# Performance work log

Measured on AMD Instinct MI355X. Metric: run time of the kernel, lower is better.

The kernel has to match this reference:

```python
import jax, jax.numpy as jnp
import numpy as np


def build_mask_even(kh, kw):
    # Hexnet build_masks: zero one edge column for kernel rows at odd distance
    # from the kernel center (hex neighborhood); returns even-row mask + shift.
    mask = np.ones((kh, kw), dtype=np.float32)
    center = kh // 2
    shift = -1 if center % 2 else 1
    for r in range(kh):
        if abs(center - r) % 2:
            if shift == 1:
                mask[r, -1] = 0.0
            else:
                mask[r, 0] = 0.0
    return mask, shift


def setup_inputs() -> dict:
    key = jax.random.key(0)
    k1, k2, k3 = jax.random.split(key, 3)
    x = jax.random.normal(k1, (16, 128, 128, 128), dtype=jnp.float32)  # NHWC
    kernel = jax.random.normal(k2, (3, 3, 128, 256), dtype=jnp.float32) * 0.05  # HWIO
    bias = jax.random.normal(k3, (256,), dtype=jnp.float32) * 0.05
    return {"x": x, "kernel": kernel, "bias": bias}


def _hconv(x, kernel, bias):
    kh, kw = kernel.shape[0], kernel.shape[1]
    mask_np, shift = build_mask_even(kh, kw)
    kernel_even = kernel * jnp.asarray(mask_np)[:, :, None, None]

    # Odd-row kernel: only the rows at odd distance from center, rolled along width.
    center = kh // 2
    odd_rows = [jnp.roll(kernel_even[r], shift, axis=0)
                for r in range(kh) if abs(center - r) % 2]
    kernel_odd = jnp.stack(odd_rows, axis=0)  # (n_odd, kw, Cin, F)

    dn = ("NHWC", "HWIO", "NHWC")
    strides = (2, 1)  # build() doubles the H stride
    out_even = jax.lax.conv_general_dilated(
        x, kernel_even, window_strides=strides, padding="SAME",
        dimension_numbers=dn)
    out_odd = jax.lax.conv_general_dilated(
        x[:, 1:], kernel_odd, window_strides=strides, padding="SAME",
        dimension_numbers=dn)

    # Interleave rows: even0, odd0, even1, odd1, ... (+ trailing even row if longer)
    he, ho = out_even.shape[1], out_odd.shape[1]
    hm = min(he, ho)
    b, _, w, f = out_even.shape
    out = jnp.stack([out_even[:, :hm], out_odd[:, :hm]], axis=2)
    out = out.reshape(b, 2 * hm, w, f)
    if he > ho:
        out = jnp.concatenate([out, out_even[:, -1:]], axis=1)

    return jax.nn.relu(out + bias)


def reference(x, kernel, bias):
    return _hconv(x, kernel, bias)
```

## Files before the change

### kernel.cpp

```cpp
#include <hip/hip_runtime.h>


#define N_  16
#define H_  128
#define W_  128
#define C_  128
#define F_  256
#define HP  130
#define WP  130

#define A_TILE_B   16640
#define B_SLOT_B   16384
#define B_BASE     A_TILE_B

typedef short bf16x8 __attribute__((ext_vector_type(8)));
typedef float f32x4  __attribute__((ext_vector_type(4)));

__device__ __forceinline__ unsigned int bf_bits(float f) {
  unsigned int u = __float_as_uint(f);
  return (u + 0x7FFFu + ((u >> 16) & 1u)) >> 16;
}
__device__ __forceinline__ unsigned int pack2(float a, float b) {
  return bf_bits(a) | (bf_bits(b) << 16);
}

__device__ __forceinline__ void even_tap(int ti, int& dr, int& dc, int& kr, int& kc) {
  switch (ti) {
    case 0:  dr = 0; dc = 0;  kr = 0; kc = 1; break;
    case 1:  dr = 0; dc = 1;  kr = 0; kc = 2; break;
    case 2:  dr = 1; dc = -1; kr = 1; kc = 0; break;
    case 3:  dr = 1; dc = 0;  kr = 1; kc = 1; break;
    case 4:  dr = 1; dc = 1;  kr = 1; kc = 2; break;
    case 5:  dr = 2; dc = 0;  kr = 2; kc = 1; break;
    default: dr = 2; dc = 1;  kr = 2; kc = 2; break;
  }
}

__global__ __launch_bounds__(256) void prep_xpadH(
    const float* __restrict__ x, char* __restrict__ xp) {
  long id = (long)blockIdx.x * 256 + threadIdx.x;
  const int g  = (int)(id & 7);
  const int hc = (int)((id >> 3) & 1);
  long pix = id >> 4;
  const int wp = (int)(pix % WP);
  long t = pix / WP;
  const int hh = (int)(t % HP);
  const int nn = (int)(t / HP);
  const int ww = wp - 1;
  uint4 o = make_uint4(0u, 0u, 0u, 0u);
  if (hh < H_ && ww >= 0 && ww < W_) {
    const float* s = x + (((long)(nn * H_ + hh) * W_ + ww) * C_ + hc * 64 + ((g ^ (wp & 7)) * 8));
    float4 a = *(const float4*)s;
    float4 b = *(const float4*)(s + 4);
    o.x = pack2(a.x, a.y); o.y = pack2(a.z, a.w);
    o.z = pack2(b.x, b.y); o.w = pack2(b.z, b.w);
  }
  *(uint4*)(xp + id * 16) = o;
}

__global__ __launch_bounds__(256) void prep_wt2(
    const float* __restrict__ k, char* __restrict__ wt2) {
  int id = blockIdx.x * 256 + threadIdx.x;
  if (id >= 7 * 2 * 2 * 128 * 8) return;
  const int g  = id & 7;
  const int f  = (id >> 3) & 127;
  const int ft = (id >> 10) & 1;
  const int hc = (id >> 11) & 1;
  const int ti = id >> 12;
  int dr, dc, kr, kc;
  even_tap(ti, dr, dc, kr, kc);
  const int fg = ft * 128 + f;
  const int c0 = hc * 64 + (g ^ (f & 7)) * 8;
  float v[8];
#pragma unroll
  for (int j = 0; j < 8; ++j)
    v[j] = k[((size_t)(kr * 3 + kc) * C_ + (c0 + j)) * F_ + fg];
  uint4 o;
  o.x = pack2(v[0], v[1]); o.y = pack2(v[2], v[3]);
  o.z = pack2(v[4], v[5]); o.w = pack2(v[6], v[7]);
  *(uint4*)(wt2 + (size_t)id * 16) = o;
}

__global__ __launch_bounds__(256, 3) void hconv_mfma(
    const char* __restrict__ xpadH,
    const char* __restrict__ wt2,
    const float* __restrict__ bias,
    float* __restrict__ out) {
  __shared__ __align__(16) char smem[49408];

  const int tid = threadIdx.x;
  const int bid = (blockIdx.x & 7) * 512 + (blockIdx.x >> 3);
  const int ft = bid & 1;
  const int h  = (bid >> 1) & 127;
  const int n  = bid >> 8;
  const int p  = h & 1;
  const int nsteps = p ? 8 : 14;

  const int lane = tid & 63;
  const int wid  = tid >> 6;
  const int wr   = wid >> 1;
  const int wc   = wid & 1;
  const int l16  = lane & 15;
  const int lk   = lane >> 4;

  auto step_info = [&](int s, int& dc, int& widx, int& dr, int& hc) {
    if (p == 0) {
      hc = (s >= 7);
      const int tap = hc ? s - 7 : s;
      int kr, kc; even_tap(tap, dr, dc, kr, kc);
      widx = tap;
    } else {
      hc = (s >= 4);
      const int j = s & 3;
      dr = j >> 1;
      dc = (j & 1) ? 0 : -1;
      widx = (j == 0) ? 0 : (j == 1) ? 1 : (j == 2) ? 5 : 6;
    }
  };
  auto tile_of = [&](int s) {
    if (p == 0) {
      const int hcp = (s >= 7);
      const int tap = hcp ? s - 7 : s;
      const int grp = (tap < 2) ? 0 : (tap < 5) ? 1 : 2;
      return hcp * 3 + grp;
    } else {
      return s >> 1;
    }
  };

  auto stageA = [&](int tile) {
    int dr, hc;
    if (p == 0) { hc = tile >= 3; const int g3 = hc ? tile - 3 : tile; dr = g3; }
    else        { hc = tile >= 2; dr = tile & 1; }
    const long pixb = (long)(n * HP + (h + dr)) * WP;
#pragma unroll
    for (int i = 0; i < 5; ++i) {
      const int L = i * 256 + tid;
      if (L < 1040) {
        const int wp = L >> 3, g = L & 7;
        const char* src = xpadH + ((pixb + wp) * 2 + hc) * 128 + g * 16;
        __builtin_amdgcn_global_load_lds(
            (const __attribute__((address_space(1))) void*)src,
            (__attribute__((address_space(3))) void*)((char*)smem + L * 16), 16, 0, 0);
      }
    }
  };
  auto stageB = [&](int s, int sel) {
    int dc, widx, dr, hc; step_info(s, dc, widx, dr, hc);
    const char* bsrc = wt2 + (size_t)((widx * 2 + hc) * 2 + ft) * 16384;
    char* base = (char*)smem + B_BASE + sel * B_SLOT_B;
#pragma unroll
    for (int i = 0; i < 4; ++i) {
      const int L = i * 256 + tid;
      __builtin_amdgcn_global_load_lds(
          (const __attribute__((address_space(1))) void*)(bsrc + L * 16),
          (__attribute__((address_space(3))) void*)(base + L * 16), 16, 0, 0);
    }
  };

  f32x4 acc[4][4] = {};

  stageA(0);
  stageB(0, 0);
  __syncthreads();

  int cur = 0;
  for (int s = 0; s < nsteps; ++s) {
    int dc, widx, dr, hc; step_info(s, dc, widx, dr, hc);
    const char* ab = (const char*)smem;
    const char* bb = (const char*)smem + B_BASE + cur * B_SLOT_B;

    bf16x8 af[4][2], bfr[4][2];
#pragma unroll
    for (int m = 0; m < 4; ++m) {
      const int wp = wr * 64 + m * 16 + l16 + dc + 1;
      const int key = wp & 7;
#pragma unroll
      for (int kk = 0; kk < 2; ++kk)
        af[m][kk] = *(const bf16x8*)(ab + wp * 128 + (((kk * 4 + lk) ^ key) * 16));
    }
#pragma unroll
    for (int fi = 0; fi < 4; ++fi) {
      const int fl = wc * 64 + fi * 16 + l16;
#pragma unroll
      for (int kk = 0; kk < 2; ++kk)
        bfr[fi][kk] = *(const bf16x8*)(bb + fl * 128 + (((kk * 4 + lk) ^ (fl & 7)) * 16));
    }

    if (s + 1 < nsteps) stageB(s + 1, cur ^ 1);

#pragma unroll
    for (int m = 0; m < 4; ++m)
#pragma unroll
      for (int fi = 0; fi < 4; ++fi)
#pragma unroll
        for (int kk = 0; kk < 2; ++kk)
          acc[m][fi] = __builtin_amdgcn_mfma_f32_16x16x32_bf16(
              af[m][kk], bfr[fi][kk], acc[m][fi], 0, 0, 0);

    if (s + 1 < nsteps) {
      if (tile_of(s + 1) != tile_of(s)) {
        __syncthreads();
        stageA(tile_of(s + 1));
      }
      __syncthreads();
      cur ^= 1;
    }
  }

#pragma unroll
  for (int fi = 0; fi < 4; ++fi) {
    const int f = ft * 128 + wc * 64 + fi * 16 + l16;
    const float bv = bias[f];
#pragma unroll
    for (int m = 0; m < 4; ++m) {
      const int w = wr * 64 + m * 16 + lk * 4;
      float* o = out + (((size_t)(n * H_ + h) * W_ + w) * F_ + f);
#pragma unroll
      for (int r = 0; r < 4; ++r) {
        float v = acc[m][fi][r] + bv;
        v = v > 0.f ? v : 0.f;
        o[(size_t)r * F_] = v;
      }
    }
  }
}

__device__ __forceinline__ void tap_info11(int t, int& dr, int& dc, int& kr, int& kc) {
  switch (t) {
    case 0:  dr = 0; dc = 0;  kr = 0; kc = 1; break;
    case 1:  dr = 0; dc = 1;  kr = 0; kc = 2; break;
    case 2:  dr = 1; dc = -1; kr = 1; kc = 0; break;
    case 3:  dr = 1; dc = 0;  kr = 1; kc = 1; break;
    case 4:  dr = 1; dc = 1;  kr = 1; kc = 2; break;
    case 5:  dr = 2; dc = 0;  kr = 2; kc = 1; break;
    case 6:  dr = 2; dc = 1;  kr = 2; kc = 2; break;
    case 7:  dr = 0; dc = -1; kr = 0; kc = 1; break;
    case 8:  dr = 0; dc = 0;  kr = 0; kc = 2; break;
    case 9:  dr = 1; dc = -1; kr = 2; kc = 1; break;
    default: dr = 1; dc = 0;  kr = 2; kc = 2; break;
  }
}

__global__ __launch_bounds__(256) void build_w_fb(
    const float* __restrict__ k, unsigned short* __restrict__ wt) {
  int tid = blockIdx.x * 256 + threadIdx.x;
  if (tid >= 11 * F_ * C_) return;
  int c = tid & 127;
  int f = (tid >> 7) & 255;
  int t = tid >> 15;
  int dr, dc, kr, kc;
  tap_info11(t, dr, dc, kr, kc);
  wt[tid] = (unsigned short)bf_bits(k[((kr * 3 + kc) * C_ + c) * F_ + f]);
}

__global__ __launch_bounds__(256, 3) void hconv_fb(
    const float* __restrict__ x,
    const unsigned short* __restrict__ wt,
    const float* __restrict__ bias,
    float* __restrict__ out) {
  __shared__ __align__(16) char smem_s[49152];
  const int tid = threadIdx.x;
  const int bid = (blockIdx.x & 7) * 1024 + (blockIdx.x >> 3);
  const int ft    = bid & 1;
  const int wtile = (bid >> 1) & 1;
  const int h     = (bid >> 2) & 127;
  const int n     = bid >> 9;
  const int f0 = ft * 128;
  const int w0 = wtile * 64;
  const int p  = h & 1;
  const int tap0   = p ? 7 : 0;
  const int nsteps = p ? 8 : 14;
  const int lane = tid & 63;
  const int wid  = tid >> 6;
  const int l16  = lane & 15;
  const int lk   = lane >> 4;
  const int awl = tid >> 2;
  const int ag2 = tid & 3;
  const int bfl   = tid >> 1;
  const int bhalf = tid & 1;
  float4 ar0, ar1, ar2, ar3;
  uint4  br0, br1, br2, br3;
  auto load_step = [&](int s) {
    const int tap = tap0 + (s >> 1);
    const int cc  = s & 1;
    int dr, dc, kr, kc;
    tap_info11(tap, dr, dc, kr, kc);
    const int hh = h + dr;
    const int wg = w0 + awl + dc;
    const bool av = (hh < H_) && (wg >= 0) && (wg < W_);
    if (av) {
      const float* ap = x + (((long)(n * H_ + hh) * W_ + wg) * C_ + cc * 64 + ag2 * 16);
      ar0 = *(const float4*)(ap);
      ar1 = *(const float4*)(ap + 4);
      ar2 = *(const float4*)(ap + 8);
      ar3 = *(const float4*)(ap + 12);
    } else {
      ar0 = ar1 = ar2 = ar3 = make_float4(0.f, 0.f, 0.f, 0.f);
    }
    const unsigned short* bp =
        wt + ((size_t)(tap * F_ + f0 + bfl) * C_ + cc * 64 + bhalf * 32);
    const uint4* bq = (const uint4*)bp;
    br0 = bq[0]; br1 = bq[1]; br2 = bq[2]; br3 = bq[3];
  };
  auto write_step = [&](int sel) {
    uint4 u0, u1;
    u0.x = pack2(ar0.x, ar0.y); u0.y = pack2(ar0.z, ar0.w);
    u0.z = pack2(ar1.x, ar1.y); u0.w = pack2(ar1.z, ar1.w);
    u1.x = pack2(ar2.x, ar2.y); u1.y = pack2(ar2.z, ar2.w);
    u1.z = pack2(ar3.x, ar3.y); u1.w = pack2(ar3.z, ar3.w);
    char* abase = (char*)smem_s + sel * 8192 + awl * 128;
    const int sw = awl & 7;
    *(uint4*)(abase + (((2 * ag2)     ^ sw) * 16)) = u0;
    *(uint4*)(abase + (((2 * ag2 + 1) ^ sw) * 16)) = u1;
    char* bbase = (char*)smem_s + 16384 + sel * 16384 + bfl * 128;
    const int sb = bfl & 7;
    *(uint4*)(bbase + (((bhalf * 4 + 0) ^ sb) * 16)) = br0;
    *(uint4*)(bbase + (((bhalf * 4 + 1) ^ sb) * 16)) = br1;
    *(uint4*)(bbase + (((bhalf * 4 + 2) ^ sb) * 16)) = br2;
    *(uint4*)(bbase + (((bhalf * 4 + 3) ^ sb) * 16)) = br3;
  };
  f32x4 acc[4][2] = {};
  load_step(0);
  write_step(0);
  load_step(1);
  __syncthreads();
  for (int s = 0; s < nsteps; ++s) {
    const int cur = s & 1;
    const char* ab = (const char*)smem_s + cur * 8192;
    const char* bb = (const char*)smem_s + 16384 + cur * 16384;
    bf16x8 af[4][2], bfr[2][2];
#pragma unroll
    for (int m = 0; m < 4; ++m)
#pragma unroll
      for (int kkk = 0; kkk < 2; ++kkk) {
        const int wl = m * 16 + l16;
        const int g  = (kkk * 4 + lk) ^ (wl & 7);
        af[m][kkk] = *(const bf16x8*)(ab + wl * 128 + g * 16);
      }
#pragma unroll
    for (int fi = 0; fi < 2; ++fi)
#pragma unroll
      for (int kkk = 0; kkk < 2; ++kkk) {
        const int fl = wid * 32 + fi * 16 + l16;
        const int g  = (kkk * 4 + lk) ^ (fl & 7);
        bfr[fi][kkk] = *(const bf16x8*)(bb + fl * 128 + g * 16);
      }
    if (s + 1 < nsteps) write_step(cur ^ 1);
    if (s + 2 < nsteps) load_step(s + 2);
#pragma unroll
    for (int m = 0; m < 4; ++m)
#pragma unroll
      for (int fi = 0; fi < 2; ++fi)
#pragma unroll
        for (int kkk = 0; kkk < 2; ++kkk)
          acc[m][fi] = __builtin_amdgcn_mfma_f32_16x16x32_bf16(
              af[m][kkk], bfr[fi][kkk], acc[m][fi], 0, 0, 0);
    __syncthreads();
  }
#pragma unroll
  for (int fi = 0; fi < 2; ++fi) {
    const int f = f0 + wid * 32 + fi * 16 + l16;
    const float bv = bias[f];
#pragma unroll
    for (int m = 0; m < 4; ++m) {
      const int w = w0 + m * 16 + lk * 4;
      float* o = out + (((size_t)(n * H_ + h) * W_ + w) * F_ + f);
#pragma unroll
      for (int r = 0; r < 4; ++r) {
        float v = acc[m][fi][r] + bv;
        v = v > 0.f ? v : 0.f;
        o[(size_t)r * F_] = v;
      }
    }
  }
}

extern "C" void kernel_launch(void* const* d_in, const int* in_sizes, int n_in,
                              void* d_out, int out_size, void* d_ws, size_t ws_size,
                              hipStream_t stream) {
  const float* x    = (const float*)d_in[0];
  const float* kern = (const float*)d_in[1];
  const float* bias = (const float*)d_in[2];
  float* out = (float*)d_out;

  const size_t XPAD_BYTES = (size_t)N_ * HP * WP * 256;
  const size_t WT2_BYTES  = (size_t)7 * 2 * 2 * 128 * 8 * 16;

  if (ws_size >= XPAD_BYTES + WT2_BYTES) {
    char* xpadH = (char*)d_ws;
    char* wt2   = (char*)d_ws + XPAD_BYTES;
    prep_xpadH<<<16900, 256, 0, stream>>>(x, xpadH);
    prep_wt2<<<112, 256, 0, stream>>>(kern, wt2);
    hconv_mfma<<<N_ * H_ * 2, 256, 0, stream>>>(xpadH, wt2, bias, out);
  } else {
    unsigned short* wt = (unsigned short*)d_ws;
    build_w_fb<<<(11 * F_ * C_ + 255) / 256, 256, 0, stream>>>(kern, wt);
    hconv_fb<<<N_ * H_ * 2 * 2, 256, 0, stream>>>(x, wt, bias, out);
  }
}
```

Measured before the change: 150.7 us.

## Load weight fragments directly into registers instead of staging through LDS

The weights are re-laid out so each lane can fetch its MFMA B fragments straight from global memory into registers, which removes the double-buffered LDS weight slots and the per-step barrier. LDS use drops from about 48KB to 16KB, and the launch-bounds occupancy hint is removed. The aim is to cut LDS traffic and synchronization and to let more blocks share a CU. In exchange, the weight loads are global (mostly L2) loads issued right after the MFMAs of each step, so their latency may be exposed, and register pressure rises.

New measurement: 158.9 us. 1.05x slower.

```diff
diff --git a/kernel.cpp b/kernel.cpp
--- a/kernel.cpp
+++ b/kernel.cpp
@@ -8,10 +8,6 @@
 #define F_  256
 #define HP  130
 #define WP  130
-
-#define A_TILE_B   16640
-#define B_SLOT_B   16384
-#define B_BASE     A_TILE_B
 
 typedef short bf16x8 __attribute__((ext_vector_type(8)));
 typedef float f32x4  __attribute__((ext_vector_type(4)));
@@ -58,35 +54,33 @@
   *(uint4*)(xp + id * 16) = o;
 }
 
-__global__ __launch_bounds__(256) void prep_wt2(
-    const float* __restrict__ k, char* __restrict__ wt2) {
+__global__ __launch_bounds__(256) void prep_wtB(
+    const float* __restrict__ k, char* __restrict__ wtB) {
   int id = blockIdx.x * 256 + threadIdx.x;
-  if (id >= 7 * 2 * 2 * 128 * 8) return;
-  const int g  = id & 7;
-  const int f  = (id >> 3) & 127;
-  const int ft = (id >> 10) & 1;
+  if (id >= 7 * 2 * 8 * 256) return;
+  const int f  = id & 255;
+  const int g  = (id >> 8) & 7;
   const int hc = (id >> 11) & 1;
   const int ti = id >> 12;
   int dr, dc, kr, kc;
   even_tap(ti, dr, dc, kr, kc);
-  const int fg = ft * 128 + f;
-  const int c0 = hc * 64 + (g ^ (f & 7)) * 8;
+  const int c0 = hc * 64 + g * 8;
   float v[8];
 #pragma unroll
   for (int j = 0; j < 8; ++j)
-    v[j] = k[((size_t)(kr * 3 + kc) * C_ + (c0 + j)) * F_ + fg];
+    v[j] = k[((size_t)(kr * 3 + kc) * C_ + (c0 + j)) * F_ + f];
   uint4 o;
   o.x = pack2(v[0], v[1]); o.y = pack2(v[2], v[3]);
   o.z = pack2(v[4], v[5]); o.w = pack2(v[6], v[7]);
-  *(uint4*)(wt2 + (size_t)id * 16) = o;
-}
-
-__global__ __launch_bounds__(256, 3) void hconv_mfma(
+  *(uint4*)(wtB + (size_t)id * 16) = o;
+}
+
+__global__ __launch_bounds__(256) void hconv_mfma(
     const char* __restrict__ xpadH,
-    const char* __restrict__ wt2,
+    const char* __restrict__ wtB,
     const float* __restrict__ bias,
     float* __restrict__ out) {
-  __shared__ __align__(16) char smem[49408];
+  __shared__ __align__(16) char smem[16640];
 
   const int tid = threadIdx.x;
   const int bid = (blockIdx.x & 7) * 512 + (blockIdx.x >> 3);
@@ -130,7 +124,7 @@
 
   auto stageA = [&](int tile) {
     int dr, hc;
-    if (p == 0) { hc = tile >= 3; const int g3 = hc ? tile - 3 : tile; dr = g3; }
+    if (p == 0) { hc = tile >= 3; dr = hc ? tile - 3 : tile; }
     else        { hc = tile >= 2; dr = tile & 1; }
     const long pixb = (long)(n * HP + (h + dr)) * WP;
 #pragma unroll
@@ -145,32 +139,35 @@
       }
     }
   };
-  auto stageB = [&](int s, int sel) {
+
+  bf16x8 bR[4][2];
+  auto loadB = [&](int s) {
     int dc, widx, dr, hc; step_info(s, dc, widx, dr, hc);
-    const char* bsrc = wt2 + (size_t)((widx * 2 + hc) * 2 + ft) * 16384;
-    char* base = (char*)smem + B_BASE + sel * B_SLOT_B;
-#pragma unroll
-    for (int i = 0; i < 4; ++i) {
-      const int L = i * 256 + tid;
-      __builtin_amdgcn_global_load_lds(
-          (const __attribute__((address_space(1))) void*)(bsrc + L * 16),
-          (__attribute__((address_space(3))) void*)(base + L * 16), 16, 0, 0);
-    }
+    const char* lanep = wtB + ((size_t)((widx * 2 + hc) * 8 + lk) * 256
+                               + ft * 128 + wc * 64 + l16) * 16;
+#pragma unroll
+    for (int fi = 0; fi < 4; ++fi)
+#pragma unroll
+      for (int kk = 0; kk < 2; ++kk)
+        bR[fi][kk] = *(const bf16x8*)(lanep + ((size_t)kk * 4 * 256 + fi * 16) * 16);
   };
 
   f32x4 acc[4][4] = {};
 
   stageA(0);
-  stageB(0, 0);
+  loadB(0);
   __syncthreads();
 
-  int cur = 0;
   for (int s = 0; s < nsteps; ++s) {
     int dc, widx, dr, hc; step_info(s, dc, widx, dr, hc);
+    if (s > 0 && tile_of(s) != tile_of(s - 1)) {
+      __syncthreads();
+      stageA(tile_of(s));
+      __syncthreads();
+    }
+
     const char* ab = (const char*)smem;
-    const char* bb = (const char*)smem + B_BASE + cur * B_SLOT_B;
-
-    bf16x8 af[4][2], bfr[4][2];
+    bf16x8 af[4][2];
 #pragma unroll
     for (int m = 0; m < 4; ++m) {
       const int wp = wr * 64 + m * 16 + l16 + dc + 1;
@@ -179,15 +176,6 @@
       for (int kk = 0; kk < 2; ++kk)
         af[m][kk] = *(const bf16x8*)(ab + wp * 128 + (((kk * 4 + lk) ^ key) * 16));
     }
-#pragma unroll
-    for (int fi = 0; fi < 4; ++fi) {
-      const int fl = wc * 64 + fi * 16 + l16;
-#pragma unroll
-      for (int kk = 0; kk < 2; ++kk)
-        bfr[fi][kk] = *(const bf16x8*)(bb + fl * 128 + (((kk * 4 + lk) ^ (fl & 7)) * 16));
-    }
-
-    if (s + 1 < nsteps) stageB(s + 1, cur ^ 1);
 
 #pragma unroll
     for (int m = 0; m < 4; ++m)
@@ -196,16 +184,9 @@
 #pragma unroll
         for (int kk = 0; kk < 2; ++kk)
           acc[m][fi] = __builtin_amdgcn_mfma_f32_16x16x32_bf16(
-              af[m][kk], bfr[fi][kk], acc[m][fi], 0, 0, 0);
-
-    if (s + 1 < nsteps) {
-      if (tile_of(s + 1) != tile_of(s)) {
-        __syncthreads();
-        stageA(tile_of(s + 1));
-      }
-      __syncthreads();
-      cur ^= 1;
-    }
+              af[m][kk], bR[fi][kk], acc[m][fi], 0, 0, 0);
+
+    if (s + 1 < nsteps) loadB(s + 1);
   }
 
 #pragma unroll
@@ -385,14 +366,14 @@
   float* out = (float*)d_out;
 
   const size_t XPAD_BYTES = (size_t)N_ * HP * WP * 256;
-  const size_t WT2_BYTES  = (size_t)7 * 2 * 2 * 128 * 8 * 16;
-
-  if (ws_size >= XPAD_BYTES + WT2_BYTES) {
+  const size_t WTB_BYTES  = (size_t)7 * 2 * 8 * 256 * 16;
+
+  if (ws_size >= XPAD_BYTES + WTB_BYTES) {
     char* xpadH = (char*)d_ws;
-    char* wt2   = (char*)d_ws + XPAD_BYTES;
+    char* wtB   = (char*)d_ws + XPAD_BYTES;
     prep_xpadH<<<16900, 256, 0, stream>>>(x, xpadH);
-    prep_wt2<<<112, 256, 0, stream>>>(kern, wt2);
-    hconv_mfma<<<N_ * H_ * 2, 256, 0, stream>>>(xpadH, wt2, bias, out);
+    prep_wtB<<<(7 * 2 * 8 * 256 + 255) / 256, 256, 0, stream>>>(kern, wtB);
+    hconv_mfma<<<N_ * H_ * 2, 256, 0, stream>>>(xpadH, wtB, bias, out);
   } else {
     unsigned short* wt = (unsigned short*)d_ws;
     build_w_fb<<<(11 * F_ * C_ + 255) / 256, 256, 0, stream>>>(kern, wt);
```

## Fuse input bf16 conversion and padding into conv kernel with register prefetch

Applied to the files above, without the earlier changes.

Removes the separate prep kernel that wrote a padded bf16 copy of the input to workspace. The conv kernel now reads fp32 input directly, handles the zero padding itself, converts to bf16, and writes the result to LDS. The next A tile is prefetched into registers while the current tile is consumed, replacing the async global-to-LDS copies. This saves a full pass over the input plus the padded buffer traffic. In exchange it adds register pressure (40 floats) and twice the global read bytes per tile, and each block repeats the conversion for rows shared with other blocks.

Result: slower. 359.2 us (+138.4%).

```diff
diff --git a/kernel.cpp b/kernel.cpp
--- a/kernel.cpp
+++ b/kernel.cpp
@@ -6,8 +6,6 @@
 #define W_  128
 #define C_  128
 #define F_  256
-#define HP  130
-#define WP  130
 
 #define A_TILE_B   16640
 #define B_SLOT_B   16384
@@ -34,28 +32,6 @@
     case 5:  dr = 2; dc = 0;  kr = 2; kc = 1; break;
     default: dr = 2; dc = 1;  kr = 2; kc = 2; break;
   }
-}
-
-__global__ __launch_bounds__(256) void prep_xpadH(
-    const float* __restrict__ x, char* __restrict__ xp) {
-  long id = (long)blockIdx.x * 256 + threadIdx.x;
-  const int g  = (int)(id & 7);
-  const int hc = (int)((id >> 3) & 1);
-  long pix = id >> 4;
-  const int wp = (int)(pix % WP);
-  long t = pix / WP;
-  const int hh = (int)(t % HP);
-  const int nn = (int)(t / HP);
-  const int ww = wp - 1;
-  uint4 o = make_uint4(0u, 0u, 0u, 0u);
-  if (hh < H_ && ww >= 0 && ww < W_) {
-    const float* s = x + (((long)(nn * H_ + hh) * W_ + ww) * C_ + hc * 64 + ((g ^ (wp & 7)) * 8));
-    float4 a = *(const float4*)s;
-    float4 b = *(const float4*)(s + 4);
-    o.x = pack2(a.x, a.y); o.y = pack2(a.z, a.w);
-    o.z = pack2(b.x, b.y); o.w = pack2(b.z, b.w);
-  }
-  *(uint4*)(xp + id * 16) = o;
 }
 
 __global__ __launch_bounds__(256) void prep_wt2(
@@ -82,7 +58,7 @@
 }
 
 __global__ __launch_bounds__(256, 3) void hconv_mfma(
-    const char* __restrict__ xpadH,
+    const float* __restrict__ x,
     const char* __restrict__ wt2,
     const float* __restrict__ bias,
     float* __restrict__ out) {
@@ -95,6 +71,7 @@
   const int n  = bid >> 8;
   const int p  = h & 1;
   const int nsteps = p ? 8 : 14;
+  const int ntiles = p ? 4 : 6;
 
   const int lane = tid & 63;
   const int wid  = tid >> 6;
@@ -128,23 +105,45 @@
     }
   };
 
-  auto stageA = [&](int tile) {
+  float4 fa[10];
+  auto loadA = [&](int tile) {
+    if (tile >= ntiles) return;
     int dr, hc;
-    if (p == 0) { hc = tile >= 3; const int g3 = hc ? tile - 3 : tile; dr = g3; }
+    if (p == 0) { hc = tile >= 3; dr = hc ? tile - 3 : tile; }
     else        { hc = tile >= 2; dr = tile & 1; }
-    const long pixb = (long)(n * HP + (h + dr)) * WP;
+    const int hh = h + dr;
+#pragma unroll
+    for (int i = 0; i < 5; ++i) {
+      const int L = i * 256 + tid;
+      fa[2 * i]     = make_float4(0.f, 0.f, 0.f, 0.f);
+      fa[2 * i + 1] = make_float4(0.f, 0.f, 0.f, 0.f);
+      if (L < 1040) {
+        const int wp = L >> 3, g = L & 7;
+        const int ww = wp - 1;
+        if (hh < H_ && ww >= 0 && ww < W_) {
+          const float* s = x + (((long)(n * H_ + hh) * W_ + ww) * C_
+                                + hc * 64 + ((g ^ (wp & 7)) * 8));
+          fa[2 * i]     = *(const float4*)s;
+          fa[2 * i + 1] = *(const float4*)(s + 4);
+        }
+      }
+    }
+  };
+  auto writeA = [&]() {
 #pragma unroll
     for (int i = 0; i < 5; ++i) {
       const int L = i * 256 + tid;
       if (L < 1040) {
-        const int wp = L >> 3, g = L & 7;
-        const char* src = xpadH + ((pixb + wp) * 2 + hc) * 128 + g * 16;
-        __builtin_amdgcn_global_load_lds(
-            (const __attribute__((address_space(1))) void*)src,
-            (__attribute__((address_space(3))) void*)((char*)smem + L * 16), 16, 0, 0);
-      }
-    }
-  };
+        uint4 u;
+        u.x = pack2(fa[2 * i].x,     fa[2 * i].y);
+        u.y = pack2(fa[2 * i].z,     fa[2 * i].w);
+        u.z = pack2(fa[2 * i + 1].x, fa[2 * i + 1].y);
+        u.w = pack2(fa[2 * i + 1].z, fa[2 * i + 1].w);
+        *(uint4*)((char*)smem + L * 16) = u;
+      }
+    }
+  };
+
   auto stageB = [&](int s, int sel) {
     int dc, widx, dr, hc; step_info(s, dc, widx, dr, hc);
     const char* bsrc = wt2 + (size_t)((widx * 2 + hc) * 2 + ft) * 16384;
@@ -160,13 +159,22 @@
 
   f32x4 acc[4][4] = {};
 
-  stageA(0);
+  loadA(0);
+  writeA();
   stageB(0, 0);
+  loadA(1);
   __syncthreads();
 
   int cur = 0;
   for (int s = 0; s < nsteps; ++s) {
     int dc, widx, dr, hc; step_info(s, dc, widx, dr, hc);
+    if (s > 0 && tile_of(s) != tile_of(s - 1)) {
+      __syncthreads();
+      writeA();
+      loadA(tile_of(s) + 1);
+      __syncthreads();
+    }
+
     const char* ab = (const char*)smem;
     const char* bb = (const char*)smem + B_BASE + cur * B_SLOT_B;
 
@@ -199,10 +207,6 @@
               af[m][kk], bfr[fi][kk], acc[m][fi], 0, 0, 0);
 
     if (s + 1 < nsteps) {
-      if (tile_of(s + 1) != tile_of(s)) {
-        __syncthreads();
-        stageA(tile_of(s + 1));
-      }
       __syncthreads();
       cur ^= 1;
     }
@@ -384,15 +388,12 @@
   const float* bias = (const float*)d_in[2];
   float* out = (float*)d_out;
 
-  const size_t XPAD_BYTES = (size_t)N_ * HP * WP * 256;
-  const size_t WT2_BYTES  = (size_t)7 * 2 * 2 * 128 * 8 * 16;
-
-  if (ws_size >= XPAD_BYTES + WT2_BYTES) {
-    char* xpadH = (char*)d_ws;
-    char* wt2   = (char*)d_ws + XPAD_BYTES;
-    prep_xpadH<<<16900, 256, 0, stream>>>(x, xpadH);
+  const size_t WT2_BYTES = (size_t)7 * 2 * 2 * 128 * 8 * 16;
+
+  if (ws_size >= WT2_BYTES) {
+    char* wt2 = (char*)d_ws;
     prep_wt2<<<112, 256, 0, stream>>>(kern, wt2);
-    hconv_mfma<<<N_ * H_ * 2, 256, 0, stream>>>(xpadH, wt2, bias, out);
+    hconv_mfma<<<N_ * H_ * 2, 256, 0, stream>>>(x, wt2, bias, out);
   } else {
     unsigned short* wt = (unsigned short*)d_ws;
     build_w_fb<<<(11 * F_ * C_ + 255) / 256, 256, 0, stream>>>(kern, wt);
```

## Compute even and odd output rows in one block sharing staged tiles

Applied to the files above, without the earlier changes.

Each 512-thread block now produces an even/odd pair of output rows. Two wave groups share the staged input row tiles and the per-tap weight slices, where before separate blocks handled each parity and each loaded its own weights and input rows. This is meant to halve weight traffic and reuse input rows across the pair. In exchange, odd-parity waves sit idle on taps they do not use, all blocks run 14 uniform steps, and dynamic shared memory grows to about 66 KB, which may reduce occupancy.

After: 366.8 us. 143% more time.

```diff
diff --git a/kernel.cpp b/kernel.cpp
--- a/kernel.cpp
+++ b/kernel.cpp
@@ -11,7 +11,7 @@
 
 #define A_TILE_B   16640
 #define B_SLOT_B   16384
-#define B_BASE     A_TILE_B
+#define B_BASE     (2 * A_TILE_B)
 
 typedef short bf16x8 __attribute__((ext_vector_type(8)));
 typedef float f32x4  __attribute__((ext_vector_type(4)));
@@ -81,133 +81,128 @@
   *(uint4*)(wt2 + (size_t)id * 16) = o;
 }
 
-__global__ __launch_bounds__(256, 3) void hconv_mfma(
+__global__ __launch_bounds__(512, 4) void hconv_mfma(
     const char* __restrict__ xpadH,
     const char* __restrict__ wt2,
     const float* __restrict__ bias,
     float* __restrict__ out) {
-  __shared__ __align__(16) char smem[49408];
+  extern __shared__ __align__(16) char smem[];
 
   const int tid = threadIdx.x;
-  const int bid = (blockIdx.x & 7) * 512 + (blockIdx.x >> 3);
+  const int bid = (blockIdx.x & 7) * 256 + (blockIdx.x >> 3);
   const int ft = bid & 1;
-  const int h  = (bid >> 1) & 127;
-  const int n  = bid >> 8;
-  const int p  = h & 1;
-  const int nsteps = p ? 8 : 14;
+  const int hp = (bid >> 1) & 63;
+  const int n  = bid >> 7;
 
   const int lane = tid & 63;
   const int wid  = tid >> 6;
-  const int wr   = wid >> 1;
+  const int par  = wid >> 2;
+  const int wr   = (wid >> 1) & 1;
   const int wc   = wid & 1;
   const int l16  = lane & 15;
   const int lk   = lane >> 4;
 
-  auto step_info = [&](int s, int& dc, int& widx, int& dr, int& hc) {
-    if (p == 0) {
-      hc = (s >= 7);
-      const int tap = hc ? s - 7 : s;
-      int kr, kc; even_tap(tap, dr, dc, kr, kc);
-      widx = tap;
-    } else {
-      hc = (s >= 4);
-      const int j = s & 3;
-      dr = j >> 1;
-      dc = (j & 1) ? 0 : -1;
-      widx = (j == 0) ? 0 : (j == 1) ? 1 : (j == 2) ? 5 : 6;
-    }
-  };
-  auto tile_of = [&](int s) {
-    if (p == 0) {
-      const int hcp = (s >= 7);
-      const int tap = hcp ? s - 7 : s;
-      const int grp = (tap < 2) ? 0 : (tap < 5) ? 1 : 2;
-      return hcp * 3 + grp;
-    } else {
-      return s >> 1;
-    }
-  };
-
-  auto stageA = [&](int tile) {
-    int dr, hc;
-    if (p == 0) { hc = tile >= 3; const int g3 = hc ? tile - 3 : tile; dr = g3; }
-    else        { hc = tile >= 2; dr = tile & 1; }
-    const long pixb = (long)(n * HP + (h + dr)) * WP;
-#pragma unroll
-    for (int i = 0; i < 5; ++i) {
-      const int L = i * 256 + tid;
+  auto stageA = [&](int row, int hc, int slot) {
+    const long pixb = (long)(n * HP + (2 * hp + row)) * WP;
+    char* base = (char*)smem + slot * A_TILE_B;
+#pragma unroll
+    for (int i = 0; i < 3; ++i) {
+      const int L = i * 512 + tid;
       if (L < 1040) {
         const int wp = L >> 3, g = L & 7;
         const char* src = xpadH + ((pixb + wp) * 2 + hc) * 128 + g * 16;
         __builtin_amdgcn_global_load_lds(
             (const __attribute__((address_space(1))) void*)src,
-            (__attribute__((address_space(3))) void*)((char*)smem + L * 16), 16, 0, 0);
+            (__attribute__((address_space(3))) void*)(base + L * 16), 16, 0, 0);
       }
     }
   };
   auto stageB = [&](int s, int sel) {
-    int dc, widx, dr, hc; step_info(s, dc, widx, dr, hc);
-    const char* bsrc = wt2 + (size_t)((widx * 2 + hc) * 2 + ft) * 16384;
+    const int tap = (s < 7) ? s : s - 7;
+    const int hc  = (s >= 7);
+    const char* bsrc = wt2 + (size_t)((tap * 2 + hc) * 2 + ft) * 16384;
     char* base = (char*)smem + B_BASE + sel * B_SLOT_B;
 #pragma unroll
-    for (int i = 0; i < 4; ++i) {
-      const int L = i * 256 + tid;
+    for (int i = 0; i < 2; ++i) {
+      const int L = i * 512 + tid;
       __builtin_amdgcn_global_load_lds(
           (const __attribute__((address_space(1))) void*)(bsrc + L * 16),
           (__attribute__((address_space(3))) void*)(base + L * 16), 16, 0, 0);
     }
   };
+  auto phase_of = [&](int s) { const int tap = (s < 7) ? s : s - 7; return (tap < 2) ? 1 : 2; };
 
   f32x4 acc[4][4] = {};
 
-  stageA(0);
+  stageA(0, 0, 0);
+  stageA(1, 0, 1);
   stageB(0, 0);
   __syncthreads();
 
   int cur = 0;
-  for (int s = 0; s < nsteps; ++s) {
-    int dc, widx, dr, hc; step_info(s, dc, widx, dr, hc);
-    const char* ab = (const char*)smem;
+  for (int s = 0; s < 14; ++s) {
+    const int tap = (s < 7) ? s : s - 7;
+    const int hc  = (s >= 7);
+
+    int row, dc, act;
+    if (par == 0) {
+      int kr, kc; even_tap(tap, row, dc, kr, kc);
+      act = 1;
+    } else {
+      act = (tap <= 1) || (tap >= 5);
+      row = (tap < 2) ? 1 : 2;
+      dc  = (tap == 0 || tap == 5) ? -1 : 0;
+    }
+    const int slot = (row == 1) ? 1 : 0;
+    const char* ab = (const char*)smem + slot * A_TILE_B;
     const char* bb = (const char*)smem + B_BASE + cur * B_SLOT_B;
 
     bf16x8 af[4][2], bfr[4][2];
-#pragma unroll
-    for (int m = 0; m < 4; ++m) {
-      const int wp = wr * 64 + m * 16 + l16 + dc + 1;
-      const int key = wp & 7;
-#pragma unroll
-      for (int kk = 0; kk < 2; ++kk)
-        af[m][kk] = *(const bf16x8*)(ab + wp * 128 + (((kk * 4 + lk) ^ key) * 16));
-    }
-#pragma unroll
-    for (int fi = 0; fi < 4; ++fi) {
-      const int fl = wc * 64 + fi * 16 + l16;
-#pragma unroll
-      for (int kk = 0; kk < 2; ++kk)
-        bfr[fi][kk] = *(const bf16x8*)(bb + fl * 128 + (((kk * 4 + lk) ^ (fl & 7)) * 16));
-    }
-
-    if (s + 1 < nsteps) stageB(s + 1, cur ^ 1);
-
-#pragma unroll
-    for (int m = 0; m < 4; ++m)
-#pragma unroll
-      for (int fi = 0; fi < 4; ++fi)
+    if (act) {
+#pragma unroll
+      for (int m = 0; m < 4; ++m) {
+        const int wp = wr * 64 + m * 16 + l16 + dc + 1;
+        const int key = wp & 7;
 #pragma unroll
         for (int kk = 0; kk < 2; ++kk)
-          acc[m][fi] = __builtin_amdgcn_mfma_f32_16x16x32_bf16(
-              af[m][kk], bfr[fi][kk], acc[m][fi], 0, 0, 0);
-
-    if (s + 1 < nsteps) {
-      if (tile_of(s + 1) != tile_of(s)) {
+          af[m][kk] = *(const bf16x8*)(ab + wp * 128 + (((kk * 4 + lk) ^ key) * 16));
+      }
+#pragma unroll
+      for (int fi = 0; fi < 4; ++fi) {
+        const int fl = wc * 64 + fi * 16 + l16;
+#pragma unroll
+        for (int kk = 0; kk < 2; ++kk)
+          bfr[fi][kk] = *(const bf16x8*)(bb + fl * 128 + (((kk * 4 + lk) ^ (fl & 7)) * 16));
+      }
+    }
+
+    if (s + 1 < 14) stageB(s + 1, cur ^ 1);
+
+    if (act) {
+#pragma unroll
+      for (int m = 0; m < 4; ++m)
+#pragma unroll
+        for (int fi = 0; fi < 4; ++fi)
+#pragma unroll
+          for (int kk = 0; kk < 2; ++kk)
+            acc[m][fi] = __builtin_amdgcn_mfma_f32_16x16x32_bf16(
+                af[m][kk], bfr[fi][kk], acc[m][fi], 0, 0, 0);
+    }
+
+    if (s + 1 < 14) {
+      const bool hcb = (s == 6);
+      const bool phb = phase_of(s + 1) != phase_of(s);
+      if (hcb || phb) {
         __syncthreads();
-        stageA(tile_of(s + 1));
+        if (hcb) { stageA(0, 1, 0); stageA(1, 1, 1); }
+        else     { stageA(2, hc, 0); }
       }
       __syncthreads();
       cur ^= 1;
     }
   }
 
+  const int hout = 2 * hp + par;
 #pragma unroll
   for (int fi = 0; fi < 4; ++fi) {
     const int f = ft * 128 + wc * 64 + fi * 16 + l16;
@@ -215,7 +210,7 @@
 #pragma unroll
     for (int m = 0; m < 4; ++m) {
       const int w = wr * 64 + m * 16 + lk * 4;
-      float* o = out + (((size_t)(n * H_ + h) * W_ + w) * F_ + f);
+      float* o = out + (((size_t)(n * H_ + hout) * W_ + w) * F_ + f);
 #pragma unroll
       for (int r = 0; r < 4; ++r) {
         float v = acc[m][fi][r] + bv;
@@ -386,13 +381,17 @@
 
   const size_t XPAD_BYTES = (size_t)N_ * HP * WP * 256;
   const size_t WT2_BYTES  = (size_t)7 * 2 * 2 * 128 * 8 * 16;
+  const int    SMEM_MAIN  = 2 * 16640 + 2 * 16384;
 
   if (ws_size >= XPAD_BYTES + WT2_BYTES) {
     char* xpadH = (char*)d_ws;
     char* wt2   = (char*)d_ws + XPAD_BYTES;
+    (void)hipFuncSetAttribute((const void*)hconv_mfma,
+                              hipFuncAttributeMaxDynamicSharedMemorySize,
+                              SMEM_MAIN);
     prep_xpadH<<<16900, 256, 0, stream>>>(x, xpadH);
     prep_wt2<<<112, 256, 0, stream>>>(kern, wt2);
-    hconv_mfma<<<N_ * H_ * 2, 256, 0, stream>>>(xpadH, wt2, bias, out);
+    hconv_mfma<<<N_ * 64 * 2, 512, SMEM_MAIN, stream>>>(xpadH, wt2, bias, out);
   } else {
     unsigned short* wt = (unsigned short*)d_ws;
     build_w_fb<<<(11 * F_ * C_ + 255) / 256, 256, 0, stream>>>(kern, wt);
```
